# Optimization experiments

Hardware: AMD Instinct MI355X
Metric: run time of the kernel (lower is better)

The kernel has to match this reference:

```python
import jax, jax.numpy as jnp
import numpy as np
from jax import lax

B, N, K, M, NC = 64, 1024, 20, 256, 40  # clouds, points/cloud, knn k, fps points (ratio 0.25), classes
EPS = 1e-5


def setup_inputs() -> dict:
    key = jax.random.key(0)
    ks = jax.random.split(key, 6)
    w = lambda k, s: jax.random.normal(k, s, jnp.float32) * 0.05
    return {
        "pos": jax.random.normal(ks[0], (B * N, 3), jnp.float32),
        "w1": w(ks[1], (64, 3)), "b1": jnp.zeros(64, jnp.float32),
        "g1": jnp.ones(64, jnp.float32), "be1": jnp.zeros(64, jnp.float32),
        "w2": w(ks[2], (64, 64)), "b2": jnp.zeros(64, jnp.float32),
        "g2": jnp.ones(64, jnp.float32), "be2": jnp.zeros(64, jnp.float32),
        "w_nn1": w(ks[3], (512, 64)), "b_nn1": jnp.zeros(512, jnp.float32),
        "g_bn2": jnp.ones(512, jnp.float32), "be_bn2": jnp.zeros(512, jnp.float32),
        "w_nn4": w(ks[4], (NC, 512)), "b_nn4": jnp.zeros(NC, jnp.float32),
    }


def _knn_idx(p):  # p: [N,3] -> [N,K] neighbor indices, self excluded (loop=False)
    d = jnp.sum(p * p, -1)[:, None] + jnp.sum(p * p, -1)[None, :] - 2.0 * (p @ p.T)
    d = d.at[jnp.arange(N), jnp.arange(N)].set(jnp.inf)
    _, idx = lax.top_k(-d, K)
    return idx


def _fps_idx(p):  # p: [N,3] -> [M] farthest-point-sampling indices (deterministic start at 0)
    def step(carry, _):
        dist, last = carry
        d = jnp.sum((p - p[last]) ** 2, -1)
        dist = jnp.minimum(dist, d)
        nxt = jnp.argmax(dist).astype(jnp.int32)
        return (dist, nxt), nxt
    init = (jnp.full((N,), 1e38, jnp.float32), jnp.int32(0))
    _, idxs = lax.scan(step, init, None, length=M - 1)
    return jnp.concatenate([jnp.zeros((1,), jnp.int32), idxs])


def _bn(x, g, b, axes):  # batch-norm with batch statistics (training mode)
    m = jnp.mean(x, axes, keepdims=True)
    v = jnp.var(x, axes, keepdims=True)
    return (x - m) * lax.rsqrt(v + EPS) * g + b


def reference(pos, w1, b1, g1, be1, w2, b2, g2, be2,
              w_nn1, b_nn1, g_bn2, be_bn2, w_nn4, b_nn4):
    p = pos.reshape(B, N, 3)
    idx = jax.vmap(_knn_idx)(p)                     # [B,N,K]
    nbr = jax.vmap(lambda pb, ib: pb[ib])(p, idx)   # [B,N,K,3]
    rel = nbr - p[:, :, None, :]                    # edge features (relative positions)
    h = jax.nn.relu(jnp.einsum('bnkc,fc->bnkf', rel, w1) + b1)
    h = _bn(h, g1, be1, (0, 1, 2))
    h = jax.nn.relu(jnp.einsum('bnkf,gf->bnkg', h, w2) + b2)
    h = _bn(h, g2, be2, (0, 1, 2))
    feat = jnp.max(h, axis=2)                       # [B,N,64] edge-conv max aggregation
    fidx = jax.vmap(_fps_idx)(p)                    # [B,M]
    f = jnp.take_along_axis(feat, fidx[:, :, None], axis=1)  # [B,M,64]
    y = jnp.einsum('bmf,hf->bmh', f, w_nn1) + b_nn1  # [B,M,512]
    y = jnp.max(y, axis=1)                           # [B,512]
    y = jax.nn.relu(y)
    y = _bn(y, g_bn2, be_bn2, (0,))
    y = y @ w_nn4.T + b_nn4                          # [B,40]
    return jax.nn.log_softmax(y, axis=1)
```

## Files before the change

### kernel.cpp

```cpp
#include <hip/hip_runtime.h>
#include <hip/hip_bf16.h>
#include <cfloat>
#include <math.h>

#define BB 64
#define NN 1024
#define KNN 20
#define MM 256
#define CC 64
#define HH 512
#define NCLS 40
#define EPSF 1e-5f
#define CNT1 (BB*NN*KNN)

#define FPS_R1 201

#define IDX_OFF    0
#define MAXH2_OFF  (IDX_OFF + BB*NN*KNN)
#define FIDX_OFF   (MAXH2_OFF + BB*NN*CC)
#define Y_OFF      (FIDX_OFF + BB*MM)
#define ACC_OFF    (Y_OFF + BB*HH)
#define W2T_OFF    (ACC_OFF + 256)
#define B2F_OFF    (W2T_OFF + CC*CC)
#define FPSD_OFF   (B2F_OFF + CC)
#define FPSC_OFF   (FPSD_OFF + BB*NN)

typedef __attribute__((ext_vector_type(8)))  short short8;
typedef __attribute__((ext_vector_type(16))) float f32x16;

static __device__ __forceinline__ unsigned short f2bf(float f) {
  unsigned u = __float_as_uint(f);
  unsigned r = (u + 0x7fffu + ((u >> 16) & 1u)) >> 16;
  return (unsigned short)r;
}

static __device__ __forceinline__ unsigned fenc(float f) {
  unsigned b = __float_as_uint(f);
  return b ^ ((unsigned)((int)b >> 31) | 0x80000000u);
}
static __device__ __forceinline__ float fdec(unsigned e) {
  return __uint_as_float((e & 0x80000000u) ? (e & 0x7FFFFFFFu) : ~e);
}

static __device__ __forceinline__ int mbcnt64(unsigned long long m) {
  return (int)__builtin_amdgcn_mbcnt_hi((unsigned)(m >> 32),
           __builtin_amdgcn_mbcnt_lo((unsigned)m, 0));
}

static __device__ __forceinline__ void knn_emit_f(const float* dq, unsigned phi, int cntHi,
                                                  int* op, int* nbr, int lane) {
  float tsf = fdec((phi << 16) | 0xFFFFu);
  if (cntHi == KNN) {
    int base = 0;
#pragma unroll
    for (int q = 0; q < 16; ++q) {
      bool pred = (dq[q] <= tsf);
      unsigned long long mask = __ballot((int)pred);
      if (pred) {
        int p_ = base + mbcnt64(mask);
        op[p_] = q*64 + lane;
        nbr[p_] = q*64 + lane;
      }
      base += (int)__popcll(mask);
    }
  } else {
    unsigned lo2 = phi << 16, hi2 = (phi << 16) | 0xFFFFu;
    while (lo2 < hi2) {
      unsigned mid = lo2 + ((hi2 - lo2) >> 1);
      float mf = fdec(mid);
      int cnt = 0;
#pragma unroll
      for (int q = 0; q < 16; ++q)
        cnt += (int)__popcll(__ballot(dq[q] <= mf));
      if (cnt >= KNN) hi2 = mid; else lo2 = mid + 1;
    }
    float xsf = fdec(lo2);
    int base = 0;
#pragma unroll
    for (int q = 0; q < 16; ++q) {
      bool pred = (dq[q] < xsf);
      unsigned long long mask = __ballot((int)pred);
      if (pred) {
        int p_ = base + mbcnt64(mask);
        op[p_] = q*64 + lane;
        nbr[p_] = q*64 + lane;
      }
      base += (int)__popcll(mask);
    }
    for (int q = 0; q < 16 && base < KNN; ++q) {
      bool pred = (dq[q] == xsf);
      unsigned long long mask = __ballot((int)pred);
      if (pred) {
        int p_ = base + mbcnt64(mask);
        if (p_ < KNN) { op[p_] = q*64 + lane; nbr[p_] = q*64 + lane; }
      }
      base += (int)__popcll(mask);
    }
  }
}

static __device__ __forceinline__ void fps_phase(
    const float* sx, const float* sy, const float* sz,
    float* fpsd, int* fpsc, int* fidxg, int b, int mStart, int mEnd) {
  int lane = threadIdx.x;
  float lx[16], ly[16], lz[16], dist[16];
#pragma unroll
  for (int q = 0; q < 16; ++q) {
    int j = q*64 + lane;
    lx[q] = sx[j]; ly[q] = sy[j]; lz[q] = sz[j];
  }
  int cur;
  if (mStart <= 1) {
#pragma unroll
    for (int q = 0; q < 16; ++q) dist[q] = 1e38f;
    if (lane == 0) fidxg[b*MM] = 0;
    cur = 0;
  } else {
#pragma unroll
    for (int q = 0; q < 16; ++q) dist[q] = fpsd[b*NN + q*64 + lane];
    cur = fpsc[b];
  }
  for (int m = mStart; m < mEnd; ++m) {
    float cpx = sx[cur], cpy = sy[cur], cpz = sz[cur];
#pragma unroll
    for (int q = 0; q < 16; ++q) {
      float dx = __fsub_rn(lx[q], cpx);
      float dy = __fsub_rn(ly[q], cpy);
      float dz = __fsub_rn(lz[q], cpz);
      float dd = __fadd_rn(__fadd_rn(__fmul_rn(dx,dx), __fmul_rn(dy,dy)), __fmul_rn(dz,dz));
      dist[q] = fminf(dist[q], dd);
    }
    float t8[8];
#pragma unroll
    for (int q = 0; q < 8; ++q) t8[q] = fmaxf(dist[q], dist[q + 8]);
#pragma unroll
    for (int q = 0; q < 4; ++q) t8[q] = fmaxf(t8[q], t8[q + 4]);
    float r = fmaxf(fmaxf(t8[0], t8[1]), fmaxf(t8[2], t8[3]));
#define FPS_VMAX_STEP(C) { \
    int tt = __builtin_amdgcn_update_dpp(__float_as_int(r), __float_as_int(r), (C), 0xf, 0xf, false); \
    r = fmaxf(r, __int_as_float(tt)); }
    FPS_VMAX_STEP(0x111)
    FPS_VMAX_STEP(0x112)
    FPS_VMAX_STEP(0x114)
    FPS_VMAX_STEP(0x118)
    FPS_VMAX_STEP(0x142)
    FPS_VMAX_STEP(0x143)
#undef FPS_VMAX_STEP
    float wmax = __int_as_float(__builtin_amdgcn_readlane(__float_as_int(r), 63));
    unsigned ci = 0xFFFFFFFFu;
#pragma unroll
    for (int q = 15; q >= 0; --q)
      if (dist[q] == wmax) ci = (unsigned)(q*64 + lane);
#define FPS_IMIN_STEP(C) { \
    unsigned tt = (unsigned)__builtin_amdgcn_update_dpp((int)ci, (int)ci, (C), 0xf, 0xf, false); \
    ci = (tt < ci) ? tt : ci; }
    FPS_IMIN_STEP(0x111)
    FPS_IMIN_STEP(0x112)
    FPS_IMIN_STEP(0x114)
    FPS_IMIN_STEP(0x118)
    FPS_IMIN_STEP(0x142)
    FPS_IMIN_STEP(0x143)
#undef FPS_IMIN_STEP
    cur = (int)(unsigned)__builtin_amdgcn_readlane((int)ci, 63);
    if (lane == 0) fidxg[b*MM + m] = cur;
  }
  if (mEnd < MM) {
#pragma unroll
    for (int q = 0; q < 16; ++q) fpsd[b*NN + q*64 + lane] = dist[q];
    if (lane == 0) fpsc[b] = cur;
  }
}

__global__ __launch_bounds__(256) void knn_fps_kernel(const float* __restrict__ pos,
                                                      int* __restrict__ idxg,
                                                      int* __restrict__ fidxg,
                                                      float* __restrict__ fpsd,
                                                      int* __restrict__ fpsc,
                                                      const float* __restrict__ w1,
                                                      const float* __restrict__ b1,
                                                      float* __restrict__ acc1) {
  __shared__ float4 pj[NN];
  __shared__ int nbrs[4][2][KNN];
  __shared__ float red[4][CC];
  if (blockIdx.x >= BB) {
    int blk = blockIdx.x - BB;
    int b  = blk >> 5;
    int nb = blk & 31;
    const float* pb = pos + (size_t)b * NN * 3;
    for (int i = threadIdx.x; i < NN; i += 256) {
      float x = pb[i*3+0], y = pb[i*3+1], z = pb[i*3+2];
      pj[i] = make_float4(x, y, z, (x*x + y*y) + z*z);
    }
    __syncthreads();
    int lane = threadIdx.x & 63;
    int wv   = threadIdx.x >> 6;
    float w1x = w1[lane*3+0], w1y = w1[lane*3+1], w1z = w1[lane*3+2], b1c = b1[lane];
    float s = 0.f, ss = 0.f;

    for (int t = 0; t < 4; ++t) {
      int iA = nb*32 + wv*8 + 2*t;
      int iB = iA + 1;
      float4 piA = pj[iA];
      float4 piB = pj[iB];
      float dA[16], dB[16];
#pragma unroll
      for (int q = 0; q < 16; ++q) {
        int j = q*64 + lane;
        float4 pw = pj[j];
        float a = piA.w + pw.w - 2.0f*(piA.x*pw.x + piA.y*pw.y + piA.z*pw.z);
        float bb2 = piB.w + pw.w - 2.0f*(piB.x*pw.x + piB.y*pw.y + piB.z*pw.z);
        if (j == iA) a = FLT_MAX;
        if (j == iB) bb2 = FLT_MAX;
        dA[q] = a; dB[q] = bb2;
      }
      float lminA = dA[0], lminB = dB[0];
#pragma unroll
      for (int q = 1; q < 16; ++q) {
        lminA = fminf(lminA, dA[q]);
        lminB = fminf(lminB, dB[q]);
      }
      float rminA = lminA, rmaxA = lminA, rminB = lminB, rmaxB = lminB;
#define KNN_DPP_STEP(C) { \
      int t1 = __builtin_amdgcn_update_dpp(__float_as_int(rminA), __float_as_int(rminA), (C), 0xf, 0xf, false); \
      int t2 = __builtin_amdgcn_update_dpp(__float_as_int(rmaxA), __float_as_int(rmaxA), (C), 0xf, 0xf, false); \
      int t3 = __builtin_amdgcn_update_dpp(__float_as_int(rminB), __float_as_int(rminB), (C), 0xf, 0xf, false); \
      int t4 = __builtin_amdgcn_update_dpp(__float_as_int(rmaxB), __float_as_int(rmaxB), (C), 0xf, 0xf, false); \
      rminA = fminf(rminA, __int_as_float(t1)); rmaxA = fmaxf(rmaxA, __int_as_float(t2)); \
      rminB = fminf(rminB, __int_as_float(t3)); rmaxB = fmaxf(rmaxB, __int_as_float(t4)); }
      KNN_DPP_STEP(0x111)
      KNN_DPP_STEP(0x112)
      KNN_DPP_STEP(0x114)
      KNN_DPP_STEP(0x118)
      KNN_DPP_STEP(0x142)
      KNN_DPP_STEP(0x143)
#undef KNN_DPP_STEP
      unsigned ploA = ((unsigned)__builtin_amdgcn_readlane((int)fenc(rminA), 63)) >> 16;
      unsigned phiA = ((unsigned)__builtin_amdgcn_readlane((int)fenc(rmaxA), 63)) >> 16;
      unsigned ploB = ((unsigned)__builtin_amdgcn_readlane((int)fenc(rminB), 63)) >> 16;
      unsigned phiB = ((unsigned)__builtin_amdgcn_readlane((int)fenc(rmaxB), 63)) >> 16;
      int cntHiA = -1, cntHiB = -1;
      while (ploA < phiA || ploB < phiB) {
        unsigned pmA = (ploA + phiA) >> 1, pmB = (ploB + phiB) >> 1;
        float tfA = fdec((pmA << 16) | 0xFFFFu);
        float tfB = fdec((pmB << 16) | 0xFFFFu);
        int cA0 = 0, cA1 = 0, cB0 = 0, cB1 = 0;
#pragma unroll
        for (int q = 0; q < 8; ++q) {
          cA0 += (int)__popcll(__ballot(dA[q] <= tfA));
          cB0 += (int)__popcll(__ballot(dB[q] <= tfB));
          cA1 += (int)__popcll(__ballot(dA[q+8] <= tfA));
          cB1 += (int)__popcll(__ballot(dB[q+8] <= tfB));
        }
        int cA = cA0 + cA1, cB = cB0 + cB1;
        if (ploA < phiA) { if (cA >= KNN) { phiA = pmA; cntHiA = cA; } else ploA = pmA + 1; }
        if (ploB < phiB) { if (cB >= KNN) { phiB = pmB; cntHiB = cB; } else ploB = pmB + 1; }
      }
      float tsA = fdec((phiA << 16) | 0xFFFFu);
      float tsB = fdec((phiB << 16) | 0xFFFFu);
      if (cntHiA < 0 || cntHiB < 0) {
        int cA = 0, cB = 0;
#pragma unroll
        for (int q = 0; q < 16; ++q) {
          cA += (int)__popcll(__ballot(dA[q] <= tsA));
          cB += (int)__popcll(__ballot(dB[q] <= tsB));
        }
        if (cntHiA < 0) cntHiA = cA;
        if (cntHiB < 0) cntHiB = cB;
      }
      int* opA = idxg + (size_t)(b*NN + iA) * KNN;
      int* opB = idxg + (size_t)(b*NN + iB) * KNN;
      int* nbA = &nbrs[wv][0][0];
      int* nbB = &nbrs[wv][1][0];
      if (cntHiA == KNN && cntHiB == KNN) {
        int baseA = 0, baseB = 0;
#pragma unroll
        for (int q = 0; q < 16; ++q) {
          bool pA = (dA[q] <= tsA);
          unsigned long long mA = __ballot((int)pA);
          bool pB = (dB[q] <= tsB);
          unsigned long long mB = __ballot((int)pB);
          if (pA) { int p_ = baseA + mbcnt64(mA); opA[p_] = q*64 + lane; nbA[p_] = q*64 + lane; }
          if (pB) { int p_ = baseB + mbcnt64(mB); opB[p_] = q*64 + lane; nbB[p_] = q*64 + lane; }
          baseA += (int)__popcll(mA);
          baseB += (int)__popcll(mB);
        }
      } else {
        knn_emit_f(dA, phiA, cntHiA, opA, nbA, lane);
        knn_emit_f(dB, phiB, cntHiB, opB, nbB, lane);
      }
#pragma unroll 4
      for (int k = 0; k < KNN; ++k) {
        int j = nbA[k];
        float4 pw = pj[j];
        float h = fmaxf(fmaf(pw.x - piA.x, w1x,
                       fmaf(pw.y - piA.y, w1y,
                       fmaf(pw.z - piA.z, w1z, b1c))), 0.f);
        s += h; ss += h*h;
      }
#pragma unroll 4
      for (int k = 0; k < KNN; ++k) {
        int j = nbB[k];
        float4 pw = pj[j];
        float h = fmaxf(fmaf(pw.x - piB.x, w1x,
                       fmaf(pw.y - piB.y, w1y,
                       fmaf(pw.z - piB.z, w1z, b1c))), 0.f);
        s += h; ss += h*h;
      }
    }
    red[wv][lane] = s; __syncthreads();
    if (wv == 0) atomicAdd(&acc1[lane], red[0][lane]+red[1][lane]+red[2][lane]+red[3][lane]);
    __syncthreads();
    red[wv][lane] = ss; __syncthreads();
    if (wv == 0) atomicAdd(&acc1[64+lane], red[0][lane]+red[1][lane]+red[2][lane]+red[3][lane]);
  } else {
    int b = blockIdx.x;
    float* base = (float*)pj;
    float* sx = base; float* sy = base + NN; float* sz = base + 2*NN;
    const float* pb = pos + (size_t)b * NN * 3;
    for (int i = threadIdx.x; i < NN; i += 256) {
      sx[i] = pb[i*3+0]; sy[i] = pb[i*3+1]; sz[i] = pb[i*3+2];
    }
    __syncthreads();
    if (threadIdx.x >= 64) return;
    fps_phase(sx, sy, sz, fpsd, fpsc, fidxg, b, 1, FPS_R1);
  }
}

__global__ void fold1_kernel(const float* __restrict__ acc, const float* __restrict__ g1,
    const float* __restrict__ be1, const float* __restrict__ w2, const float* __restrict__ b2,
    unsigned short* __restrict__ w2bf, float* __restrict__ b2f) {
  __shared__ float s1[CC], t1[CC];
  int tid = threadIdx.x;
  if (tid < CC) {
    float cnt = (float)CNT1;
    float m = acc[tid] / cnt;
    float v = acc[64+tid] / cnt - m*m;
    float sc = g1[tid] * rsqrtf(v + EPSF);
    s1[tid] = sc; t1[tid] = be1[tid] - m*sc;
  }
  __syncthreads();
  int frag = tid >> 6;
  int lane = tid & 63;
  int nt = frag >> 2, ks = frag & 3;
  int cout = nt*32 + (lane & 31);
  int cin0 = ks*16 + (lane >> 5)*8;
  for (int j = 0; j < 8; ++j) {
    int cin = cin0 + j;
    w2bf[((size_t)frag*64 + lane)*8 + j] = f2bf(w2[cout*CC + cin] * s1[cin]);
  }
  if (tid < CC) {
    float accb = b2[tid];
    for (int ci = 0; ci < CC; ++ci) accb += t1[ci]*w2[tid*CC + ci];
    b2f[tid] = accb;
  }
}

__global__ __launch_bounds__(256, 4) void conv2_kernel(const float* __restrict__ pos,
    const int* __restrict__ idxg, const float* __restrict__ w1, const float* __restrict__ b1,
    const unsigned short* __restrict__ w2bf, const float* __restrict__ b2fg,
    float* __restrict__ maxh2, float* __restrict__ acc2,
    int* __restrict__ fidxg, float* __restrict__ fpsd, int* __restrict__ fpsc) {
  __shared__ float px[NN], py[NN], pz[NN];
  __shared__ float4 relw[4][KNN];
  __shared__ __align__(16) unsigned short h1s[4][2112];
  __shared__ float redbuf[4][2*CC];
  if (blockIdx.x < BB) {
    int b = blockIdx.x;
    const float* pb = pos + (size_t)b*NN*3;
    for (int i = threadIdx.x; i < NN; i += 256) {
      px[i] = pb[i*3+0]; py[i] = pb[i*3+1]; pz[i] = pb[i*3+2];
    }
    __syncthreads();
    if (threadIdx.x >= 64) return;
    fps_phase(px, py, pz, fpsd, fpsc, fidxg, b, FPS_R1, MM);
    return;
  }
  int blk = blockIdx.x - BB;
  int b = blk >> 4;
  int nb = blk & 15;
  const float* pb = pos + (size_t)b*NN*3;
  for (int i = threadIdx.x; i < NN; i += 256) {
    px[i] = pb[i*3+0]; py[i] = pb[i*3+1]; pz[i] = pb[i*3+2];
  }
  int lane = threadIdx.x & 63, w = threadIdx.x >> 6;
  int half = lane >> 5, l31 = lane & 31;
  short8 Bf[2][4];
#pragma unroll
  for (int nt = 0; nt < 2; ++nt)
#pragma unroll
    for (int ks = 0; ks < 4; ++ks)
      Bf[nt][ks] = *(const short8*)&w2bf[((size_t)(nt*4+ks)*64 + lane)*8];
  float b2o0 = b2fg[l31], b2o1 = b2fg[32 + l31];
  float w1x = w1[lane*3+0], w1y = w1[lane*3+1], w1z = w1[lane*3+2], b1c = b1[lane];
  unsigned short* hw = h1s[w];
  {
    short8 zz = {0,0,0,0,0,0,0,0};
    for (int z = lane; z < 96; z += 64) {
      int g = z / 12, r = 20 + z % 12;
      *(short8*)&hw[g*264 + r*8] = zz;
    }
  }
  float sA = 0.f, ssA = 0.f, sB = 0.f, ssB = 0.f;
  int nxt = 0;
  {
    int n0 = nb*64 + w*16;
    if (lane < KNN) nxt = idxg[(size_t)(b*NN + n0)*KNN + lane];
  }
  __syncthreads();
  for (int t = 0; t < 16; ++t) {
    int n = nb*64 + w*16 + t;
    if (lane < KNN) {
      int j = nxt;
      relw[w][lane] = make_float4(px[j]-px[n], py[j]-py[n], pz[j]-pz[n], 0.f);
      if (t < 15) nxt = idxg[(size_t)(b*NN + n + 1)*KNN + lane];
    }
    int gbase = (lane >> 3)*264 + (lane & 7);
#pragma unroll
    for (int k = 0; k < KNN; ++k) {
      float4 r4 = relw[w][k];
      float h = fmaxf(fmaf(r4.x, w1x, fmaf(r4.y, w1y, fmaf(r4.z, w1z, b1c))), 0.f);
      hw[gbase + k*8] = f2bf(h);
    }
    f32x16 acc0 = {}; f32x16 acc1 = {};
#pragma unroll
    for (int ks = 0; ks < 4; ++ks) {
      short8 A = *(const short8*)&hw[(ks*2 + half)*264 + l31*8];
      acc0 = __builtin_amdgcn_mfma_f32_32x32x16_bf16(A, Bf[0][ks], acc0, 0, 0, 0);
      acc1 = __builtin_amdgcn_mfma_f32_32x32x16_bf16(A, Bf[1][ks], acc1, 0, 0, 0);
    }
    float mx0 = 0.f, mx1 = 0.f;
#pragma unroll
    for (int reg = 0; reg < 8; ++reg) {
      float v0 = fmaxf(acc0[reg] + b2o0, 0.f);
      float v1 = fmaxf(acc1[reg] + b2o1, 0.f);
      sA += v0; ssA += v0*v0; sB += v1; ssB += v1*v1;
      mx0 = fmaxf(mx0, v0); mx1 = fmaxf(mx1, v1);
    }
    if (half == 0) {
#pragma unroll
      for (int reg = 8; reg < 12; ++reg) {
        float v0 = fmaxf(acc0[reg] + b2o0, 0.f);
        float v1 = fmaxf(acc1[reg] + b2o1, 0.f);
        sA += v0; ssA += v0*v0; sB += v1; ssB += v1*v1;
        mx0 = fmaxf(mx0, v0); mx1 = fmaxf(mx1, v1);
      }
    }
    mx0 = fmaxf(mx0, __shfl_xor(mx0, 32, 64));
    mx1 = fmaxf(mx1, __shfl_xor(mx1, 32, 64));
    if (half == 0) {
      float* mp = maxh2 + (size_t)(b*NN + n)*CC;
      mp[l31] = mx0; mp[32 + l31] = mx1;
    }
  }
  sA += __shfl_xor(sA, 32, 64); ssA += __shfl_xor(ssA, 32, 64);
  sB += __shfl_xor(sB, 32, 64); ssB += __shfl_xor(ssB, 32, 64);
  if (half == 0) { redbuf[w][l31] = sA; redbuf[w][32 + l31] = sB; }
  __syncthreads();
  if (w == 0) atomicAdd(&acc2[lane], redbuf[0][lane]+redbuf[1][lane]+redbuf[2][lane]+redbuf[3][lane]);
  __syncthreads();
  if (half == 0) { redbuf[w][l31] = ssA; redbuf[w][32 + l31] = ssB; }
  __syncthreads();
  if (w == 0) atomicAdd(&acc2[64+lane], redbuf[0][lane]+redbuf[1][lane]+redbuf[2][lane]+redbuf[3][lane]);
}

__global__ __launch_bounds__(256) void head_kernel(const float* __restrict__ maxh2,
    const int* __restrict__ fidxg, const float* __restrict__ acc2,
    const float* __restrict__ g2, const float* __restrict__ be2,
    const float* __restrict__ wnn1, const float* __restrict__ bnn1, float* __restrict__ Y) {
  int b = blockIdx.x >> 2;
  int hc = blockIdx.x & 3;
  __shared__ __align__(16) float ftile[128][CC];
  __shared__ float red2[4][128];
  __shared__ float s2s[CC], t2s[CC];
  if (threadIdx.x < CC) {
    int c = threadIdx.x;
    float cnt = (float)CNT1;
    float m = acc2[c]/cnt;
    float v = acc2[64+c]/cnt - m*m;
    float sc = g2[c]*rsqrtf(v+EPSF);
    s2s[c] = sc;
    t2s[c] = be2[c] - m*sc;
  }
  int hl = threadIdx.x & 63, mseg = threadIdx.x >> 6;
  int hA = hc*128 + hl, hB = hA + 64;
  float4 wva[16], wvb[16];
  const float4* wrA = (const float4*)(wnn1 + (size_t)hA*CC);
  const float4* wrB = (const float4*)(wnn1 + (size_t)hB*CC);
#pragma unroll
  for (int q = 0; q < 16; ++q) { wva[q] = wrA[q]; wvb[q] = wrB[q]; }
  float bestA = -FLT_MAX, bestB = -FLT_MAX;
  const int* fb = fidxg + b*MM;
  __syncthreads();
  for (int chunk = 0; chunk < 2; ++chunk) {
    {
      int row = threadIdx.x & 127, chal = threadIdx.x >> 7;
      int fi = fb[chunk*128 + row];
      const float* src = maxh2 + (size_t)(b*NN + fi)*CC;
      for (int ci = chal*32; ci < chal*32+32; ++ci)
        ftile[row][ci] = s2s[ci]*src[ci] + t2s[ci];
    }
    __syncthreads();
    for (int m = mseg*32; m < mseg*32+32; ++m) {
      float accA = 0.f, accB = 0.f;
#pragma unroll
      for (int cq = 0; cq < 16; ++cq) {
        float4 f = *((const float4*)&ftile[m][cq*4]);
        accA = fmaf(f.x, wva[cq].x, accA);
        accA = fmaf(f.y, wva[cq].y, accA);
        accA = fmaf(f.z, wva[cq].z, accA);
        accA = fmaf(f.w, wva[cq].w, accA);
        accB = fmaf(f.x, wvb[cq].x, accB);
        accB = fmaf(f.y, wvb[cq].y, accB);
        accB = fmaf(f.z, wvb[cq].z, accB);
        accB = fmaf(f.w, wvb[cq].w, accB);
      }
      bestA = fmaxf(bestA, accA);
      bestB = fmaxf(bestB, accB);
    }
    __syncthreads();
  }
  red2[mseg][hl] = bestA;
  red2[mseg][64 + hl] = bestB;
  __syncthreads();
  if (threadIdx.x < 128) {
    int hh = hc*128 + threadIdx.x;
    float v = fmaxf(fmaxf(red2[0][threadIdx.x], red2[1][threadIdx.x]),
                    fmaxf(red2[2][threadIdx.x], red2[3][threadIdx.x])) + bnn1[hh];
    Y[(size_t)b*HH + hh] = fmaxf(v, 0.f);
  }
}

__global__ __launch_bounds__(256) void logits_kernel(const float* __restrict__ Y,
    const float* __restrict__ g3, const float* __restrict__ be3,
    const float* __restrict__ w4, const float* __restrict__ b4, float* __restrict__ out) {
  int b = blockIdx.x;
  __shared__ float ybn[HH];
  __shared__ float s3s[HH], t3s[HH];
  __shared__ float lg[NCLS];
  __shared__ float lse;
  for (int h = threadIdx.x; h < HH; h += 256) {
    float s = 0.f;
    for (int bb = 0; bb < BB; ++bb) s += Y[(size_t)bb*HH + h];
    float m = s / (float)BB;
    float v = 0.f;
    for (int bb = 0; bb < BB; ++bb) { float d = Y[(size_t)bb*HH + h] - m; v += d*d; }
    v /= (float)BB;
    float sc = g3[h] * rsqrtf(v + EPSF);
    s3s[h] = sc; t3s[h] = be3[h] - m*sc;
  }
  __syncthreads();
  for (int hh = threadIdx.x; hh < HH; hh += 256)
    ybn[hh] = Y[(size_t)b*HH + hh]*s3s[hh] + t3s[hh];
  __syncthreads();
  if (threadIdx.x < NCLS) {
    int j = threadIdx.x;
    float acc = b4[j];
    const float* wr = w4 + (size_t)j*HH;
    for (int ci = 0; ci < HH; ++ci) acc = fmaf(ybn[ci], wr[ci], acc);
    lg[j] = acc;
  }
  __syncthreads();
  if (threadIdx.x == 0) {
    float mx = -FLT_MAX;
    for (int j = 0; j < NCLS; ++j) mx = fmaxf(mx, lg[j]);
    float s = 0.f;
    for (int j = 0; j < NCLS; ++j) s += expf(lg[j] - mx);
    lse = mx + logf(s);
  }
  __syncthreads();
  if (threadIdx.x < NCLS) out[b*NCLS + threadIdx.x] = lg[threadIdx.x] - lse;
}

extern "C" void kernel_launch(void* const* d_in, const int* in_sizes, int n_in,
                              void* d_out, int out_size, void* d_ws, size_t ws_size,
                              hipStream_t stream) {
  const float* pos  = (const float*)d_in[0];
  const float* w1   = (const float*)d_in[1];
  const float* b1   = (const float*)d_in[2];
  const float* g1   = (const float*)d_in[3];
  const float* be1  = (const float*)d_in[4];
  const float* w2   = (const float*)d_in[5];
  const float* b2   = (const float*)d_in[6];
  const float* g2   = (const float*)d_in[7];
  const float* be2  = (const float*)d_in[8];
  const float* wnn1 = (const float*)d_in[9];
  const float* bnn1 = (const float*)d_in[10];
  const float* gbn2 = (const float*)d_in[11];
  const float* bebn2= (const float*)d_in[12];
  const float* wnn4 = (const float*)d_in[13];
  const float* bnn4 = (const float*)d_in[14];
  float* ws = (float*)d_ws;
  int*   idxg  = (int*)(ws + IDX_OFF);
  float* maxh2 = ws + MAXH2_OFF;
  int*   fidxg = (int*)(ws + FIDX_OFF);
  float* Y     = ws + Y_OFF;
  float* acc1  = ws + ACC_OFF;
  float* acc2  = ws + ACC_OFF + 128;
  unsigned short* w2bf = (unsigned short*)(ws + W2T_OFF);
  float* b2f   = ws + B2F_OFF;
  float* fpsd  = ws + FPSD_OFF;
  int*   fpsc  = (int*)(ws + FPSC_OFF);
  float* outp  = (float*)d_out;

  hipMemsetAsync((void*)(ws + ACC_OFF), 0, 256*sizeof(float), stream);
  knn_fps_kernel<<<BB + BB*32, 256, 0, stream>>>(pos, idxg, fidxg, fpsd, fpsc, w1, b1, acc1);
  fold1_kernel<<<1, 512, 0, stream>>>(acc1, g1, be1, w2, b2, w2bf, b2f);
  conv2_kernel<<<BB + BB*16, 256, 0, stream>>>(pos, idxg, w1, b1, w2bf, b2f, maxh2, acc2, fidxg, fpsd, fpsc);
  head_kernel<<<BB*4, 256, 0, stream>>>(maxh2, fidxg, acc2, g2, be2, wnn1, bnn1, Y);
  logits_kernel<<<BB, 256, 0, stream>>>(Y, gbn2, bebn2, wnn4, bnn4, outp);
}
```

Before: 333.0 us.

## Run full FPS in knn kernel and fold BN1 via last-block ticket

FPS now runs all 255 steps inside the knn kernel instead of splitting at step 201 and resuming in the conv2 kernel, which removes the save/restore of distance state. The separate fold1 kernel is removed: the last knn block, found through an atomic ticket counter, computes the BN1 fold of w2/b2. This saves one launch and the FPS state traffic. The cost is that the long serial FPS chain can now extend the knn kernel's critical path, since it no longer overlaps with conv2.

```diff
diff --git a/kernel.cpp b/kernel.cpp
--- a/kernel.cpp
+++ b/kernel.cpp
@@ -13,17 +13,14 @@
 #define EPSF 1e-5f
 #define CNT1 (BB*NN*KNN)
 
-#define FPS_R1 201
-
 #define IDX_OFF    0
 #define MAXH2_OFF  (IDX_OFF + BB*NN*KNN)
 #define FIDX_OFF   (MAXH2_OFF + BB*NN*CC)
 #define Y_OFF      (FIDX_OFF + BB*MM)
 #define ACC_OFF    (Y_OFF + BB*HH)
-#define W2T_OFF    (ACC_OFF + 256)
+#define TICKET_OFF (ACC_OFF + 256)
+#define W2T_OFF    (TICKET_OFF + 4)
 #define B2F_OFF    (W2T_OFF + CC*CC)
-#define FPSD_OFF   (B2F_OFF + CC)
-#define FPSC_OFF   (FPSD_OFF + BB*NN)
 
 typedef __attribute__((ext_vector_type(8)))  short short8;
 typedef __attribute__((ext_vector_type(16))) float f32x16;
@@ -99,28 +96,20 @@
   }
 }
 
-static __device__ __forceinline__ void fps_phase(
+static __device__ __forceinline__ void fps_full(
     const float* sx, const float* sy, const float* sz,
-    float* fpsd, int* fpsc, int* fidxg, int b, int mStart, int mEnd) {
+    int* fidxg, int b) {
   int lane = threadIdx.x;
   float lx[16], ly[16], lz[16], dist[16];
 #pragma unroll
   for (int q = 0; q < 16; ++q) {
     int j = q*64 + lane;
     lx[q] = sx[j]; ly[q] = sy[j]; lz[q] = sz[j];
-  }
-  int cur;
-  if (mStart <= 1) {
-#pragma unroll
-    for (int q = 0; q < 16; ++q) dist[q] = 1e38f;
-    if (lane == 0) fidxg[b*MM] = 0;
-    cur = 0;
-  } else {
-#pragma unroll
-    for (int q = 0; q < 16; ++q) dist[q] = fpsd[b*NN + q*64 + lane];
-    cur = fpsc[b];
-  }
-  for (int m = mStart; m < mEnd; ++m) {
+    dist[q] = 1e38f;
+  }
+  if (lane == 0) fidxg[b*MM] = 0;
+  int cur = 0;
+  for (int m = 1; m < MM; ++m) {
     float cpx = sx[cur], cpy = sy[cur], cpz = sz[cur];
 #pragma unroll
     for (int q = 0; q < 16; ++q) {
@@ -164,24 +153,26 @@
     cur = (int)(unsigned)__builtin_amdgcn_readlane((int)ci, 63);
     if (lane == 0) fidxg[b*MM + m] = cur;
   }
-  if (mEnd < MM) {
-#pragma unroll
-    for (int q = 0; q < 16; ++q) fpsd[b*NN + q*64 + lane] = dist[q];
-    if (lane == 0) fpsc[b] = cur;
-  }
 }
 
 __global__ __launch_bounds__(256) void knn_fps_kernel(const float* __restrict__ pos,
                                                       int* __restrict__ idxg,
                                                       int* __restrict__ fidxg,
-                                                      float* __restrict__ fpsd,
-                                                      int* __restrict__ fpsc,
                                                       const float* __restrict__ w1,
                                                       const float* __restrict__ b1,
-                                                      float* __restrict__ acc1) {
+                                                      float* __restrict__ acc1,
+                                                      int* __restrict__ ticket,
+                                                      const float* __restrict__ g1,
+                                                      const float* __restrict__ be1,
+                                                      const float* __restrict__ w2,
+                                                      const float* __restrict__ b2,
+                                                      unsigned short* __restrict__ w2bf,
+                                                      float* __restrict__ b2f) {
   __shared__ float4 pj[NN];
   __shared__ int nbrs[4][2][KNN];
   __shared__ float red[4][CC];
+  __shared__ float s1s[CC], t1s[CC];
+  __shared__ int amLast;
   if (blockIdx.x >= BB) {
     int blk = blockIdx.x - BB;
     int b  = blk >> 5;
@@ -312,6 +303,40 @@
     __syncthreads();
     red[wv][lane] = ss; __syncthreads();
     if (wv == 0) atomicAdd(&acc1[64+lane], red[0][lane]+red[1][lane]+red[2][lane]+red[3][lane]);
+    __syncthreads();
+    __threadfence();
+    if (threadIdx.x == 0) {
+      int prev = atomicAdd(ticket, 1);
+      amLast = (prev == BB*32 - 1);
+    }
+    __syncthreads();
+    if (!amLast) return;
+    __threadfence();
+    int tid = threadIdx.x;
+    if (tid < CC) {
+      float a0 = atomicAdd(&acc1[tid], 0.f);
+      float a1 = atomicAdd(&acc1[64+tid], 0.f);
+      float cnt = (float)CNT1;
+      float m = a0 / cnt;
+      float v = a1 / cnt - m*m;
+      float sc = g1[tid] * rsqrtf(v + EPSF);
+      s1s[tid] = sc; t1s[tid] = be1[tid] - m*sc;
+    }
+    __syncthreads();
+    for (int frag = tid >> 6; frag < 8; frag += 4) {
+      int nt = frag >> 2, ks = frag & 3;
+      int cout = nt*32 + (lane & 31);
+      int cin0 = ks*16 + (lane >> 5)*8;
+      for (int j = 0; j < 8; ++j) {
+        int cin = cin0 + j;
+        w2bf[((size_t)frag*64 + lane)*8 + j] = f2bf(w2[cout*CC + cin] * s1s[cin]);
+      }
+    }
+    if (tid < CC) {
+      float accb = b2[tid];
+      for (int ci = 0; ci < CC; ++ci) accb += t1s[ci]*w2[tid*CC + ci];
+      b2f[tid] = accb;
+    }
   } else {
     int b = blockIdx.x;
     float* base = (float*)pj;
@@ -322,62 +347,20 @@
     }
     __syncthreads();
     if (threadIdx.x >= 64) return;
-    fps_phase(sx, sy, sz, fpsd, fpsc, fidxg, b, 1, FPS_R1);
-  }
-}
-
-__global__ void fold1_kernel(const float* __restrict__ acc, const float* __restrict__ g1,
-    const float* __restrict__ be1, const float* __restrict__ w2, const float* __restrict__ b2,
-    unsigned short* __restrict__ w2bf, float* __restrict__ b2f) {
-  __shared__ float s1[CC], t1[CC];
-  int tid = threadIdx.x;
-  if (tid < CC) {
-    float cnt = (float)CNT1;
-    float m = acc[tid] / cnt;
-    float v = acc[64+tid] / cnt - m*m;
-    float sc = g1[tid] * rsqrtf(v + EPSF);
-    s1[tid] = sc; t1[tid] = be1[tid] - m*sc;
-  }
-  __syncthreads();
-  int frag = tid >> 6;
-  int lane = tid & 63;
-  int nt = frag >> 2, ks = frag & 3;
-  int cout = nt*32 + (lane & 31);
-  int cin0 = ks*16 + (lane >> 5)*8;
-  for (int j = 0; j < 8; ++j) {
-    int cin = cin0 + j;
-    w2bf[((size_t)frag*64 + lane)*8 + j] = f2bf(w2[cout*CC + cin] * s1[cin]);
-  }
-  if (tid < CC) {
-    float accb = b2[tid];
-    for (int ci = 0; ci < CC; ++ci) accb += t1[ci]*w2[tid*CC + ci];
-    b2f[tid] = accb;
+    fps_full(sx, sy, sz, fidxg, b);
   }
 }
 
 __global__ __launch_bounds__(256, 4) void conv2_kernel(const float* __restrict__ pos,
     const int* __restrict__ idxg, const float* __restrict__ w1, const float* __restrict__ b1,
     const unsigned short* __restrict__ w2bf, const float* __restrict__ b2fg,
-    float* __restrict__ maxh2, float* __restrict__ acc2,
-    int* __restrict__ fidxg, float* __restrict__ fpsd, int* __restrict__ fpsc) {
+    float* __restrict__ maxh2, float* __restrict__ acc2) {
   __shared__ float px[NN], py[NN], pz[NN];
   __shared__ float4 relw[4][KNN];
   __shared__ __align__(16) unsigned short h1s[4][2112];
   __shared__ float redbuf[4][2*CC];
-  if (blockIdx.x < BB) {
-    int b = blockIdx.x;
-    const float* pb = pos + (size_t)b*NN*3;
-    for (int i = threadIdx.x; i < NN; i += 256) {
-      px[i] = pb[i*3+0]; py[i] = pb[i*3+1]; pz[i] = pb[i*3+2];
-    }
-    __syncthreads();
-    if (threadIdx.x >= 64) return;
-    fps_phase(px, py, pz, fpsd, fpsc, fidxg, b, FPS_R1, MM);
-    return;
-  }
-  int blk = blockIdx.x - BB;
-  int b = blk >> 4;
-  int nb = blk & 15;
+  int b = blockIdx.x >> 4;
+  int nb = blockIdx.x & 15;
   const float* pb = pos + (size_t)b*NN*3;
   for (int i = threadIdx.x; i < NN; i += 256) {
     px[i] = pb[i*3+0]; py[i] = pb[i*3+1]; pz[i] = pb[i*3+2];
@@ -596,16 +579,15 @@
   float* Y     = ws + Y_OFF;
   float* acc1  = ws + ACC_OFF;
   float* acc2  = ws + ACC_OFF + 128;
+  int*   ticket= (int*)(ws + TICKET_OFF);
   unsigned short* w2bf = (unsigned short*)(ws + W2T_OFF);
   float* b2f   = ws + B2F_OFF;
-  float* fpsd  = ws + FPSD_OFF;
-  int*   fpsc  = (int*)(ws + FPSC_OFF);
   float* outp  = (float*)d_out;
 
-  hipMemsetAsync((void*)(ws + ACC_OFF), 0, 256*sizeof(float), stream);
-  knn_fps_kernel<<<BB + BB*32, 256, 0, stream>>>(pos, idxg, fidxg, fpsd, fpsc, w1, b1, acc1);
-  fold1_kernel<<<1, 512, 0, stream>>>(acc1, g1, be1, w2, b2, w2bf, b2f);
-  conv2_kernel<<<BB + BB*16, 256, 0, stream>>>(pos, idxg, w1, b1, w2bf, b2f, maxh2, acc2, fidxg, fpsd, fpsc);
+  hipMemsetAsync((void*)(ws + ACC_OFF), 0, 260*sizeof(float), stream);
+  knn_fps_kernel<<<BB + BB*32, 256, 0, stream>>>(pos, idxg, fidxg, w1, b1, acc1,
+                                                 ticket, g1, be1, w2, b2, w2bf, b2f);
+  conv2_kernel<<<BB*16, 256, 0, stream>>>(pos, idxg, w1, b1, w2bf, b2f, maxh2, acc2);
   head_kernel<<<BB*4, 256, 0, stream>>>(maxh2, fidxg, acc2, g2, be2, wnn1, bnn1, Y);
   logits_kernel<<<BB, 256, 0, stream>>>(Y, gbn2, bebn2, wnn4, bnn4, outp);
 }
```

After: 491.5 us. 1.48x slower.
